# Kernel tuning notes

Hardware: AMD Instinct MI355X
Metric: run time of the kernel (lower is better)

Reference implementation:

```python
import jax, jax.numpy as jnp
import numpy as np

NUM_HEADS = 16

def setup_inputs() -> dict:
    key = jax.random.key(0)
    ks = jax.random.split(key, 9)
    E = 1024
    T, B = 2048, 2
    s = E ** -0.5
    return {
        "query": jax.random.normal(ks[0], (T, B, E), dtype=jnp.float32),
        "Wq": jax.random.normal(ks[1], (E, E), dtype=jnp.float32) * s,
        "bq": jax.random.normal(ks[2], (E,), dtype=jnp.float32) * 0.02,
        "Wk": jax.random.normal(ks[3], (E, E), dtype=jnp.float32) * s,
        "bk": jax.random.normal(ks[4], (E,), dtype=jnp.float32) * 0.02,
        "Wv": jax.random.normal(ks[5], (E, E), dtype=jnp.float32) * s,
        "bv": jax.random.normal(ks[6], (E,), dtype=jnp.float32) * 0.02,
        "Wo": jax.random.normal(ks[7], (E, E), dtype=jnp.float32) * s,
        "bo": jax.random.normal(ks[8], (E,), dtype=jnp.float32) * 0.02,
    }

def reference(query, Wq, bq, Wk, bk, Wv, bv, Wo, bo):
    # query: [T, B, E] (seq-first, fairseq/ESM layout)
    T, B, E = query.shape
    H = NUM_HEADS
    D = E // H
    scaling = D ** -0.5
    # projections (eqx Linear: x @ W.T + b); note k/v also come from `query` (self-attention)
    q = (query @ Wq.T + bq) * scaling
    k = query @ Wk.T + bk
    v = query @ Wv.T + bv
    # [T, B, E] -> [B*H, T, D]
    q = q.reshape(T, B * H, D).transpose(1, 0, 2)
    k = k.reshape(T, B * H, D).transpose(1, 0, 2)
    v = v.reshape(T, B * H, D).transpose(1, 0, 2)
    # full score matrix [B*H, T, T], softmax in fp32 (as in original)
    scores = jnp.einsum('ntd,nsd->nts', q, k)
    attn_w = jax.nn.softmax(scores.astype(jnp.float32), axis=-1)
    attn = jnp.einsum('nts,nsd->ntd', attn_w.astype(v.dtype), v)
    # [B*H, T, D] -> [T, B, E]
    attn = attn.transpose(1, 0, 2).reshape(T, B, E)
    return attn @ Wo.T + bo
```

## Files before the change

### kernel.cpp

```cpp
#include <hip/hip_runtime.h>
#include <hip/hip_bf16.h>


typedef __attribute__((ext_vector_type(8))) short short8;
typedef __attribute__((ext_vector_type(4))) float f32x4;
typedef __attribute__((ext_vector_type(16))) float f32x16;
typedef __attribute__((ext_vector_type(4))) unsigned u32x4;

#define T_DIM 2048
#define B_DIM 2
#define E_DIM 1024
#define H_DIM 16
#define D_DIM 64
#define M_ROWS (T_DIM * B_DIM)
#define QKV_N (3 * E_DIM)
#define HEAD_ELEMS (32 * 2048 * 64)
#define LOG2E 1.44269504088896340736f

__device__ __forceinline__ unsigned short f2bf(float f) {
    unsigned u = __builtin_bit_cast(unsigned, f);
    unsigned r = (u + 0x7fffu + ((u >> 16) & 1u)) >> 16;
    return (unsigned short)r;
}

__device__ __forceinline__ unsigned cvt_pk_bf16(float lo, float hi) {
    unsigned d;
    asm("v_cvt_pk_bf16_f32 %0, %1, %2" : "=v"(d) : "v"(lo), "v"(hi));
    return d;
}

__device__ __forceinline__ float vmax16(const f32x16& v) {
    float a0 = fmaxf(v[0], v[1]),  a1 = fmaxf(v[2], v[3]);
    float a2 = fmaxf(v[4], v[5]),  a3 = fmaxf(v[6], v[7]);
    float a4 = fmaxf(v[8], v[9]),  a5 = fmaxf(v[10], v[11]);
    float a6 = fmaxf(v[12], v[13]), a7 = fmaxf(v[14], v[15]);
    float b0 = fmaxf(a0, a1), b1 = fmaxf(a2, a3);
    float b2 = fmaxf(a4, a5), b3 = fmaxf(a6, a7);
    return fmaxf(fmaxf(b0, b1), fmaxf(b2, b3));
}

__device__ __forceinline__ void gload_lds16(const void* g, void* l) {
    __builtin_amdgcn_global_load_lds(
        (const __attribute__((address_space(1))) void*)g,
        (__attribute__((address_space(3))) void*)l, 16, 0, 0);
}

__device__ __forceinline__ f32x16 mfma32(short8 a, short8 b, f32x16 c) {
    return __builtin_amdgcn_mfma_f32_32x32x16_bf16(a, b, c, 0, 0, 0);
}

__global__ __launch_bounds__(256) void cast_all(
    const float* __restrict__ X,
    const float* __restrict__ Wq, const float* __restrict__ Wk,
    const float* __restrict__ Wv, const float* __restrict__ Wo,
    unsigned short* __restrict__ Xbf,
    unsigned short* __restrict__ Wcat,
    unsigned short* __restrict__ Wobf)
{
    int idx = blockIdx.x * 256 + threadIdx.x;
    size_t base = (size_t)idx * 8;
    int row = (int)(base >> 10);
    int col = (int)(base & 1023);
    const float* src;
    unsigned short* dst;
    float scale = 1.0f;
    if (row < 4096) {
        src = X + base;
        dst = Xbf + base;
    } else if (row < 7168) {
        int wrow = row - 4096;
        if (wrow < 1024)      { src = Wq + ((size_t)wrow << 10) + col; scale = 0.125f * LOG2E; }
        else if (wrow < 2048) { src = Wk + ((size_t)(wrow - 1024) << 10) + col; }
        else                  { src = Wv + ((size_t)(wrow - 2048) << 10) + col; }
        dst = Wcat + ((size_t)wrow << 10) + col;
    } else {
        int wrow = row - 7168;
        src = Wo + ((size_t)wrow << 10) + col;
        dst = Wobf + ((size_t)wrow << 10) + col;
    }
    float4 f0 = *(const float4*)src;
    float4 f1 = *(const float4*)(src + 4);
    short8 r;
    r[0] = (short)f2bf(f0.x * scale);
    r[1] = (short)f2bf(f0.y * scale);
    r[2] = (short)f2bf(f0.z * scale);
    r[3] = (short)f2bf(f0.w * scale);
    r[4] = (short)f2bf(f1.x * scale);
    r[5] = (short)f2bf(f1.y * scale);
    r[6] = (short)f2bf(f1.z * scale);
    r[7] = (short)f2bf(f1.w * scale);
    *(short8*)dst = r;
}

__global__ __launch_bounds__(256) void bias_fuse(
    const float* __restrict__ bq, const float* __restrict__ bk,
    const float* __restrict__ bv, float* __restrict__ biasq)
{
    int i = blockIdx.x * 256 + threadIdx.x;
    if (i < 1024)       biasq[i] = 0.125f * LOG2E * bq[i];
    else if (i < 2048)  biasq[i] = bk[i - 1024];
    else if (i < 3072)  biasq[i] = bv[i - 2048];
}

template <int MODE>
__global__ __launch_bounds__(256) void gemm_bt(
    const unsigned short* __restrict__ A,
    const unsigned short* __restrict__ B,
    const float* __restrict__ bias,
    void* __restrict__ outp,
    int M, int N, int K)
{
    __shared__ alignas(16) unsigned short As[128 * 32];
    __shared__ alignas(16) unsigned short Bs[128 * 32];
    const int tid = threadIdx.x;
    const int wave = tid >> 6, lane = tid & 63;
    const int lr = lane & 15, lg = lane >> 4;
    const int nbx = N >> 7;
    const int bx = blockIdx.x % nbx, by = blockIdx.x / nbx;
    const int wr = wave >> 1, wc = wave & 1;

    f32x4 acc[4][4] = {};

    for (int kt = 0; kt < K; kt += 32) {
        for (int pass = 0; pass < 2; ++pass) {
            int c = pass * 256 + wave * 64 + lane;
            int row = c >> 2, kc = c & 3;
            const unsigned short* srcA = A + (size_t)(by * 128 + row) * K + kt + kc * 8;
            const unsigned short* srcB = B + (size_t)(bx * 128 + row) * K + kt + kc * 8;
            char* dstA = (char*)As + (pass * 256 + wave * 64) * 16;
            char* dstB = (char*)Bs + (pass * 256 + wave * 64) * 16;
            gload_lds16(srcA, dstA);
            gload_lds16(srcB, dstB);
        }
        __syncthreads();
        short8 af[4], bf[4];
#pragma unroll
        for (int m = 0; m < 4; ++m)
            af[m] = *(const short8*)&As[(wr * 64 + m * 16 + lr) * 32 + lg * 8];
#pragma unroll
        for (int n = 0; n < 4; ++n)
            bf[n] = *(const short8*)&Bs[(wc * 64 + n * 16 + lr) * 32 + lg * 8];
#pragma unroll
        for (int m = 0; m < 4; ++m)
#pragma unroll
            for (int n = 0; n < 4; ++n)
                acc[m][n] = __builtin_amdgcn_mfma_f32_16x16x32_bf16(af[m], bf[n], acc[m][n], 0, 0, 0);
        __syncthreads();
    }

    const int gcol0 = bx * 128 + wc * 64;
    const int grow0 = by * 128 + wr * 64;
    if (MODE == 0) {
        unsigned short* qb = (unsigned short*)outp;
#pragma unroll
        for (int m = 0; m < 4; ++m) {
#pragma unroll
            for (int n = 0; n < 4; ++n) {
                int col = gcol0 + n * 16 + lr;
                float bsv = bias[col];
                int which = col >> 10;
                int e = col & 1023;
                int h = e >> 6, d = e & 63;
                if (which < 2) {
                    unsigned short* bufb = qb + (size_t)which * HEAD_ELEMS;
#pragma unroll
                    for (int j = 0; j < 4; ++j) {
                        int r = grow0 + m * 16 + lg * 4 + j;
                        int t = r >> 1, b = r & 1;
                        int bh = b * 16 + h;
                        bufb[((size_t)bh * 2048 + t) * 64 + d] = f2bf(acc[m][n][j] + bsv);
                    }
                } else {
                    unsigned* vT32 = (unsigned*)(qb + (size_t)2 * HEAD_ELEMS);
                    int t0 = (grow0 + m * 16 + lg * 4) >> 1;
                    int dwidx = t0 >> 1;
                    int dwp = (dwidx & ~6) | ((dwidx & 2) << 1) | ((dwidx & 4) >> 1);
                    unsigned w0 = (unsigned)f2bf(acc[m][n][0] + bsv) |
                                  ((unsigned)f2bf(acc[m][n][2] + bsv) << 16);
                    unsigned w1 = (unsigned)f2bf(acc[m][n][1] + bsv) |
                                  ((unsigned)f2bf(acc[m][n][3] + bsv) << 16);
                    vT32[(size_t)(h * 64 + d) * 1024 + dwp] = w0;
                    vT32[(size_t)((16 + h) * 64 + d) * 1024 + dwp] = w1;
                }
            }
        }
    } else {
        float* O = (float*)outp;
#pragma unroll
        for (int m = 0; m < 4; ++m) {
#pragma unroll
            for (int n = 0; n < 4; ++n) {
                int col = gcol0 + n * 16 + lr;
                float bsv = bias[col];
#pragma unroll
                for (int j = 0; j < 4; ++j) {
                    int r = grow0 + m * 16 + lg * 4 + j;
                    O[(size_t)r * N + col] = acc[m][n][j] + bsv;
                }
            }
        }
    }
}

__global__ __launch_bounds__(256) void attn_fwd(
    const unsigned short* __restrict__ q,
    const unsigned short* __restrict__ k,
    const unsigned short* __restrict__ vT,
    unsigned short* __restrict__ outb)
{
    __shared__ alignas(16) unsigned short Ks[2][64 * 64];
    __shared__ alignas(16) unsigned short Vs[2][64 * 64];
    const int tid = threadIdx.x, wv = tid >> 6, l = tid & 63;
    const int ql = l & 31, hi = l >> 5;
    const int bh = blockIdx.x >> 4;
    const int q0 = (blockIdx.x & 15) * 128;
    const unsigned short* qh = q + (size_t)bh * (2048 * 64);
    const unsigned short* kh = k + (size_t)bh * (2048 * 64);
    const unsigned short* vh = vT + (size_t)bh * (64 * 2048);

    const int qrow = q0 + wv * 32 + ql;
    short8 qv[4];
#pragma unroll
    for (int c = 0; c < 4; ++c)
        qv[c] = *(const short8*)&qh[(size_t)qrow * 64 + c * 16 + hi * 8];

    f32x16 accO[2] = {};
    float mrun = -1e30f, lrun = 0.0f;

    auto stage = [&](int buf, int kt) {
#pragma unroll
        for (int p = 0; p < 2; ++p) {
            int c = p * 256 + tid;
            int row = c >> 3;
            int sxb = ((c & 7) * 16) ^ ((row & 7) << 4);
            gload_lds16(kh + (size_t)(kt + row) * 64 + (sxb >> 1),
                        (char*)&Ks[buf][0] + c * 16);
        }
#pragma unroll
        for (int p = 0; p < 2; ++p) {
            int c = p * 256 + tid;
            int d = c >> 3;
            int sxb = ((c & 7) * 16) ^ ((d & 7) << 4);
            gload_lds16(vh + (size_t)d * 2048 + kt + (sxb >> 1),
                        (char*)&Vs[buf][0] + c * 16);
        }
    };

    stage(0, 0);
    for (int t = 0; t < 32; ++t) {
        const int buf = t & 1;
        if (t < 31) {
            stage(buf ^ 1, (t + 1) * 64);
            asm volatile("s_waitcnt vmcnt(4)" ::: "memory");
        } else {
            asm volatile("s_waitcnt vmcnt(0)" ::: "memory");
        }
        __builtin_amdgcn_s_barrier();
        __builtin_amdgcn_sched_barrier(0);

        const char* Kb = (const char*)&Ks[buf][0];
        const char* Vb = (const char*)&Vs[buf][0];

        f32x16 st[2] = {};
        __builtin_amdgcn_s_setprio(1);
#pragma unroll
        for (int m = 0; m < 2; ++m) {
            int krow = m * 32 + ql;
#pragma unroll
            for (int c = 0; c < 4; ++c) {
                int bo = (krow * 128 + c * 32 + hi * 16) ^ ((krow & 7) << 4);
                short8 ka = *(const short8*)(Kb + bo);
                st[m] = mfma32(ka, qv[c], st[m]);
            }
        }
        __builtin_amdgcn_s_setprio(0);

        float pm = fmaxf(vmax16(st[0]), vmax16(st[1]));
        pm = fmaxf(pm, __shfl_xor(pm, 32));
        if (__any(pm > mrun + 8.0f)) {
            float mnew = fmaxf(mrun, pm);
            float scal = __builtin_amdgcn_exp2f(mrun - mnew);
            mrun = mnew;
            lrun *= scal;
#pragma unroll
            for (int n = 0; n < 2; ++n)
#pragma unroll
                for (int r = 0; r < 16; ++r) accO[n][r] *= scal;
        }
        float rs = 0.0f;
#pragma unroll
        for (int m = 0; m < 2; ++m)
#pragma unroll
            for (int r = 0; r < 16; ++r) {
                float e = __builtin_amdgcn_exp2f(st[m][r] - mrun);
                st[m][r] = e;
                rs += e;
            }
        lrun += rs + __shfl_xor(rs, 32);

        short8 pa[4];
#pragma unroll
        for (int kc = 0; kc < 4; ++kc) {
            int m = kc >> 1, b8 = (kc & 1) * 8;
            u32x4 u;
            u[0] = cvt_pk_bf16(st[m][b8 + 0], st[m][b8 + 1]);
            u[1] = cvt_pk_bf16(st[m][b8 + 2], st[m][b8 + 3]);
            u[2] = cvt_pk_bf16(st[m][b8 + 4], st[m][b8 + 5]);
            u[3] = cvt_pk_bf16(st[m][b8 + 6], st[m][b8 + 7]);
            pa[kc] = __builtin_bit_cast(short8, u);
        }

        __builtin_amdgcn_s_setprio(1);
#pragma unroll
        for (int n = 0; n < 2; ++n) {
            int d = n * 32 + ql;
#pragma unroll
            for (int kc = 0; kc < 4; ++kc) {
                int bo = (d * 128 + kc * 32 + hi * 16) ^ ((d & 7) << 4);
                short8 va = *(const short8*)(Vb + bo);
                accO[n] = mfma32(va, pa[kc], accO[n]);
            }
        }
        __builtin_amdgcn_s_setprio(0);
        __builtin_amdgcn_s_barrier();
        __builtin_amdgcn_sched_barrier(0);
    }

    const float inv = 1.0f / lrun;
    const int b = bh >> 4, h = bh & 15;
    const int orow = qrow * 2 + b;
#pragma unroll
    for (int n = 0; n < 2; ++n)
#pragma unroll
        for (int rq = 0; rq < 4; ++rq) {
            uint2 u;
            u.x = cvt_pk_bf16(accO[n][rq * 4 + 0] * inv, accO[n][rq * 4 + 1] * inv);
            u.y = cvt_pk_bf16(accO[n][rq * 4 + 2] * inv, accO[n][rq * 4 + 3] * inv);
            *(uint2*)&outb[(size_t)orow * 1024 + h * 64 + n * 32 + rq * 8 + hi * 4] = u;
        }
}

extern "C" void kernel_launch(void* const* d_in, const int* in_sizes, int n_in,
                              void* d_out, int out_size, void* d_ws, size_t ws_size,
                              hipStream_t stream) {
    const float* X  = (const float*)d_in[0];
    const float* Wq = (const float*)d_in[1];
    const float* bq = (const float*)d_in[2];
    const float* Wk = (const float*)d_in[3];
    const float* bk = (const float*)d_in[4];
    const float* Wv = (const float*)d_in[5];
    const float* bv = (const float*)d_in[6];
    const float* Wo = (const float*)d_in[7];
    const float* bo = (const float*)d_in[8];
    float* out = (float*)d_out;

    char* ws = (char*)d_ws;
    if (ws_size < ((size_t)49 << 20)) return;
    unsigned short* Xbf   = (unsigned short*)(ws);
    unsigned short* Wcat  = (unsigned short*)(ws + ((size_t)8  << 20));
    unsigned short* Wobf  = (unsigned short*)(ws + ((size_t)14 << 20));
    unsigned short* qb    = (unsigned short*)(ws + ((size_t)16 << 20));
    unsigned short* ab    = (unsigned short*)(ws + ((size_t)40 << 20));
    float*          biasq = (float*)(ws + ((size_t)48 << 20));
    unsigned short* kb  = qb + (size_t)HEAD_ELEMS;
    unsigned short* vTb = qb + (size_t)2 * HEAD_ELEMS;

    cast_all<<<4096, 256, 0, stream>>>(X, Wq, Wk, Wv, Wo, Xbf, Wcat, Wobf);
    bias_fuse<<<12, 256, 0, stream>>>(bq, bk, bv, biasq);
    gemm_bt<0><<<dim3((M_ROWS / 128) * (QKV_N / 128)), 256, 0, stream>>>(
        Xbf, Wcat, biasq, (void*)qb, M_ROWS, QKV_N, E_DIM);
    attn_fwd<<<dim3(32 * 16), 256, 0, stream>>>(qb, kb, vTb, ab);
    gemm_bt<1><<<dim3((M_ROWS / 128) * (E_DIM / 128)), 256, 0, stream>>>(
        ab, Wobf, bo, (void*)out, M_ROWS, E_DIM, E_DIM);
}
```

Measured before the change: 142.0 us.

## Software-pipeline attention so the PV MFMA of one tile overlaps the QK of the next

```diff
diff --git a/kernel.cpp b/kernel.cpp
--- a/kernel.cpp
+++ b/kernel.cpp
@@ -202,7 +202,122 @@
     }
 }
 
-__global__ __launch_bounds__(256) void attn_fwd(
+struct AttnCtx {
+    const unsigned short* kh;
+    const unsigned short* vh;
+    int tid, ql, hi;
+};
+
+template<bool DO_PV>
+__device__ __forceinline__ void attn_step(
+    const AttnCtx& cx, int t,
+    unsigned short (*Ks)[64 * 64], unsigned short (*Vs)[64 * 64],
+    const short8 (&qv)[4],
+    const short8 (&vfP)[8], const short8 (&paP)[4],
+    short8 (&vfC)[8], short8 (&paC)[4],
+    f32x16 (&accO)[2], float& mrun, float& lrun)
+{
+    const int buf = t & 1;
+    const int tid = cx.tid, ql = cx.ql, hi = cx.hi;
+    if (t < 31) {
+        const int kt = (t + 1) * 64;
+#pragma unroll
+        for (int p = 0; p < 2; ++p) {
+            int c = p * 256 + tid;
+            int row = c >> 3;
+            int sxb = ((c & 7) * 16) ^ ((row & 7) << 4);
+            gload_lds16(cx.kh + (size_t)(kt + row) * 64 + (sxb >> 1),
+                        (char*)&Ks[buf ^ 1][0] + c * 16);
+        }
+#pragma unroll
+        for (int p = 0; p < 2; ++p) {
+            int c = p * 256 + tid;
+            int d = c >> 3;
+            int sxb = ((c & 7) * 16) ^ ((d & 7) << 4);
+            gload_lds16(cx.vh + (size_t)d * 2048 + kt + (sxb >> 1),
+                        (char*)&Vs[buf ^ 1][0] + c * 16);
+        }
+        asm volatile("s_waitcnt vmcnt(4)" ::: "memory");
+    } else {
+        asm volatile("s_waitcnt vmcnt(0)" ::: "memory");
+    }
+    __builtin_amdgcn_s_barrier();
+    __builtin_amdgcn_sched_barrier(0);
+
+    const char* Kb = (const char*)&Ks[buf][0];
+    const char* Vb = (const char*)&Vs[buf][0];
+
+    f32x16 st[2] = {};
+    __builtin_amdgcn_s_setprio(1);
+#pragma unroll
+    for (int m = 0; m < 2; ++m) {
+        int krow = m * 32 + ql;
+#pragma unroll
+        for (int c = 0; c < 4; ++c) {
+            int bo = (krow * 128 + c * 32 + hi * 16) ^ ((krow & 7) << 4);
+            short8 ka = *(const short8*)(Kb + bo);
+            st[m] = mfma32(ka, qv[c], st[m]);
+        }
+    }
+#pragma unroll
+    for (int n = 0; n < 2; ++n) {
+        int d = n * 32 + ql;
+#pragma unroll
+        for (int kc = 0; kc < 4; ++kc) {
+            int bo = (d * 128 + kc * 32 + hi * 16) ^ ((d & 7) << 4);
+            vfC[n * 4 + kc] = *(const short8*)(Vb + bo);
+        }
+    }
+    if constexpr (DO_PV) {
+#pragma unroll
+        for (int n = 0; n < 2; ++n)
+#pragma unroll
+            for (int kc = 0; kc < 4; ++kc)
+                accO[n] = mfma32(vfP[n * 4 + kc], paP[kc], accO[n]);
+    }
+    __builtin_amdgcn_s_setprio(0);
+    __builtin_amdgcn_sched_barrier(0);
+
+    float pm = fmaxf(vmax16(st[0]), vmax16(st[1]));
+    pm = fmaxf(pm, __shfl_xor(pm, 32));
+    if (__any(pm > mrun + 8.0f)) {
+        float mnew = fmaxf(mrun, pm);
+        float scal = __builtin_amdgcn_exp2f(mrun - mnew);
+        mrun = mnew;
+        lrun *= scal;
+#pragma unroll
+        for (int n = 0; n < 2; ++n)
+#pragma unroll
+            for (int r = 0; r < 16; ++r) accO[n][r] *= scal;
+    }
+    float rs = 0.0f;
+#pragma unroll
+    for (int m = 0; m < 2; ++m)
+#pragma unroll
+        for (int r = 0; r < 16; ++r) {
+            float e = __builtin_amdgcn_exp2f(st[m][r] - mrun);
+            st[m][r] = e;
+            rs += e;
+        }
+    lrun += rs + __shfl_xor(rs, 32);
+
+#pragma unroll
+    for (int kc = 0; kc < 4; ++kc) {
+        int m = kc >> 1, b8 = (kc & 1) * 8;
+        u32x4 u;
+        u[0] = cvt_pk_bf16(st[m][b8 + 0], st[m][b8 + 1]);
+        u[1] = cvt_pk_bf16(st[m][b8 + 2], st[m][b8 + 3]);
+        u[2] = cvt_pk_bf16(st[m][b8 + 4], st[m][b8 + 5]);
+        u[3] = cvt_pk_bf16(st[m][b8 + 6], st[m][b8 + 7]);
+        paC[kc] = __builtin_bit_cast(short8, u);
+    }
+
+    asm volatile("s_waitcnt lgkmcnt(0)" ::: "memory");
+    __builtin_amdgcn_sched_barrier(0);
+    __builtin_amdgcn_s_barrier();
+}
+
+__global__ __launch_bounds__(256, 2) void attn_fwd(
     const unsigned short* __restrict__ q,
     const unsigned short* __restrict__ k,
     const unsigned short* __restrict__ vT,
@@ -215,8 +330,10 @@
     const int bh = blockIdx.x >> 4;
     const int q0 = (blockIdx.x & 15) * 128;
     const unsigned short* qh = q + (size_t)bh * (2048 * 64);
-    const unsigned short* kh = k + (size_t)bh * (2048 * 64);
-    const unsigned short* vh = vT + (size_t)bh * (64 * 2048);
+    AttnCtx cx;
+    cx.kh = k + (size_t)bh * (2048 * 64);
+    cx.vh = vT + (size_t)bh * (64 * 2048);
+    cx.tid = tid; cx.ql = ql; cx.hi = hi;
 
     const int qrow = q0 + wv * 32 + ql;
     short8 qv[4];
@@ -226,105 +343,38 @@
 
     f32x16 accO[2] = {};
     float mrun = -1e30f, lrun = 0.0f;
-
-    auto stage = [&](int buf, int kt) {
+    short8 vfA[8], vfB[8], paA[4], paB[4];
+
+    {
 #pragma unroll
         for (int p = 0; p < 2; ++p) {
             int c = p * 256 + tid;
             int row = c >> 3;
             int sxb = ((c & 7) * 16) ^ ((row & 7) << 4);
-            gload_lds16(kh + (size_t)(kt + row) * 64 + (sxb >> 1),
-                        (char*)&Ks[buf][0] + c * 16);
+            gload_lds16(cx.kh + (size_t)row * 64 + (sxb >> 1),
+                        (char*)&Ks[0][0] + c * 16);
         }
 #pragma unroll
         for (int p = 0; p < 2; ++p) {
             int c = p * 256 + tid;
             int d = c >> 3;
             int sxb = ((c & 7) * 16) ^ ((d & 7) << 4);
-            gload_lds16(vh + (size_t)d * 2048 + kt + (sxb >> 1),
-                        (char*)&Vs[buf][0] + c * 16);
-        }
-    };
-
-    stage(0, 0);
-    for (int t = 0; t < 32; ++t) {
-        const int buf = t & 1;
-        if (t < 31) {
-            stage(buf ^ 1, (t + 1) * 64);
-            asm volatile("s_waitcnt vmcnt(4)" ::: "memory");
-        } else {
-            asm volatile("s_waitcnt vmcnt(0)" ::: "memory");
-        }
-        __builtin_amdgcn_s_barrier();
-        __builtin_amdgcn_sched_barrier(0);
-
-        const char* Kb = (const char*)&Ks[buf][0];
-        const char* Vb = (const char*)&Vs[buf][0];
-
-        f32x16 st[2] = {};
-        __builtin_amdgcn_s_setprio(1);
-#pragma unroll
-        for (int m = 0; m < 2; ++m) {
-            int krow = m * 32 + ql;
-#pragma unroll
-            for (int c = 0; c < 4; ++c) {
-                int bo = (krow * 128 + c * 32 + hi * 16) ^ ((krow & 7) << 4);
-                short8 ka = *(const short8*)(Kb + bo);
-                st[m] = mfma32(ka, qv[c], st[m]);
-            }
-        }
-        __builtin_amdgcn_s_setprio(0);
-
-        float pm = fmaxf(vmax16(st[0]), vmax16(st[1]));
-        pm = fmaxf(pm, __shfl_xor(pm, 32));
-        if (__any(pm > mrun + 8.0f)) {
-            float mnew = fmaxf(mrun, pm);
-            float scal = __builtin_amdgcn_exp2f(mrun - mnew);
-            mrun = mnew;
-            lrun *= scal;
-#pragma unroll
-            for (int n = 0; n < 2; ++n)
-#pragma unroll
-                for (int r = 0; r < 16; ++r) accO[n][r] *= scal;
-        }
-        float rs = 0.0f;
-#pragma unroll
-        for (int m = 0; m < 2; ++m)
-#pragma unroll
-            for (int r = 0; r < 16; ++r) {
-                float e = __builtin_amdgcn_exp2f(st[m][r] - mrun);
-                st[m][r] = e;
-                rs += e;
-            }
-        lrun += rs + __shfl_xor(rs, 32);
-
-        short8 pa[4];
-#pragma unroll
-        for (int kc = 0; kc < 4; ++kc) {
-            int m = kc >> 1, b8 = (kc & 1) * 8;
-            u32x4 u;
-            u[0] = cvt_pk_bf16(st[m][b8 + 0], st[m][b8 + 1]);
-            u[1] = cvt_pk_bf16(st[m][b8 + 2], st[m][b8 + 3]);
-            u[2] = cvt_pk_bf16(st[m][b8 + 4], st[m][b8 + 5]);
-            u[3] = cvt_pk_bf16(st[m][b8 + 6], st[m][b8 + 7]);
-            pa[kc] = __builtin_bit_cast(short8, u);
-        }
-
-        __builtin_amdgcn_s_setprio(1);
-#pragma unroll
-        for (int n = 0; n < 2; ++n) {
-            int d = n * 32 + ql;
-#pragma unroll
-            for (int kc = 0; kc < 4; ++kc) {
-                int bo = (d * 128 + kc * 32 + hi * 16) ^ ((d & 7) << 4);
-                short8 va = *(const short8*)(Vb + bo);
-                accO[n] = mfma32(va, pa[kc], accO[n]);
-            }
-        }
-        __builtin_amdgcn_s_setprio(0);
-        __builtin_amdgcn_s_barrier();
-        __builtin_amdgcn_sched_barrier(0);
-    }
+            gload_lds16(cx.vh + (size_t)d * 2048 + (sxb >> 1),
+                        (char*)&Vs[0][0] + c * 16);
+        }
+    }
+
+    attn_step<false>(cx, 0, Ks, Vs, qv, vfB, paB, vfA, paA, accO, mrun, lrun);
+    for (int t = 1; t < 31; t += 2) {
+        attn_step<true>(cx, t,     Ks, Vs, qv, vfA, paA, vfB, paB, accO, mrun, lrun);
+        attn_step<true>(cx, t + 1, Ks, Vs, qv, vfB, paB, vfA, paA, accO, mrun, lrun);
+    }
+    attn_step<true>(cx, 31, Ks, Vs, qv, vfA, paA, vfB, paB, accO, mrun, lrun);
+#pragma unroll
+    for (int n = 0; n < 2; ++n)
+#pragma unroll
+        for (int kc = 0; kc < 4; ++kc)
+            accO[n] = mfma32(vfB[n * 4 + kc], paB[kc], accO[n]);
 
     const float inv = 1.0f / lrun;
     const int b = bh >> 4, h = bh & 15;
```

After: 133.2 us. 6.2% less time.
